# Performance work log

Measured on AMD Instinct MI355X. Metric: run time of the kernel, lower is better.

The kernel has to match this reference:

```python
import jax, jax.numpy as jnp
import numpy as np

B, NB, D, H = 2048, 12, 256, 16
NU, NI, NR = 100000, 100000, 6
EPS = 1e-10


def _lin(k, din, dout):
    k1, k2 = jax.random.split(k)
    s = 1.0 / np.sqrt(din)
    w = jax.random.uniform(k1, (din, dout), minval=-s, maxval=s, dtype=jnp.float32)
    b = jax.random.uniform(k2, (dout,), minval=-s, maxval=s, dtype=jnp.float32)
    return w, b


def setup_inputs() -> dict:
    key = jax.random.key(0)
    ks = jax.random.split(key, 24)
    inp = {}
    inp['iids'] = jax.random.randint(ks[0], (B,), 0, NI)
    inp['i_user_pad'] = jnp.stack([
        jax.random.randint(ks[1], (B, NB), 0, NU),
        jax.random.randint(ks[2], (B, NB), 0, NR)], axis=-1)
    inp['i_item_pad'] = jax.random.randint(ks[3], (B, NB), 0, NI)
    inp['i_item_user_pad'] = jnp.stack([
        jax.random.randint(ks[4], (B, NB, NB), 0, NI),
        jax.random.randint(ks[5], (B, NB, NB), 0, NR)], axis=-1)
    inp['user_table'] = jax.random.normal(ks[6], (NU, D), dtype=jnp.float32) * 0.02
    inp['item_table'] = jax.random.normal(ks[7], (NI, D), dtype=jnp.float32) * 0.02
    inp['rate_table'] = jax.random.normal(ks[8], (NR, D), dtype=jnp.float32) * 0.02
    # g_u: 2D -> D -> D
    inp['g_u_w1'], inp['g_u_b1'] = _lin(ks[9], 2 * D, D)
    inp['g_u_w2'], inp['g_u_b2'] = _lin(ks[10], D, D)
    # item_users_att: 2D -> D -> H
    inp['attu_w1'], inp['attu_b1'] = _lin(ks[11], 2 * D, D)
    inp['attu_w2'], inp['attu_b2'] = _lin(ks[12], D, H)
    # item_users_head: NB*H -> NB*H//2 -> NB
    inp['headu_w1'], inp['headu_b1'] = _lin(ks[13], NB * H, NB * H // 2)
    inp['headu_w2'], inp['headu_b2'] = _lin(ks[14], NB * H // 2, NB)
    # aggre_items: D -> D (+relu)
    inp['aggi_w'], inp['aggi_b'] = _lin(ks[15], D, D)
    # item_items_att: 2D -> D -> H
    inp['attii_w1'], inp['attii_b1'] = _lin(ks[16], 2 * D, D)
    inp['attii_w2'], inp['attii_b2'] = _lin(ks[17], D, H)
    # item_items_head: NB*H -> NB*H//2 -> NB
    inp['headii_w1'], inp['headii_b1'] = _lin(ks[18], NB * H, NB * H // 2)
    inp['headii_w2'], inp['headii_b2'] = _lin(ks[19], NB * H // 2, NB)
    # aggre_item2item: D -> D (+relu)
    inp['aggii_w'], inp['aggii_b'] = _lin(ks[20], D, D)
    # combine_mlp: 2D -> D -> D -> D, relu each
    inp['comb_w1'], inp['comb_b1'] = _lin(ks[21], 2 * D, D)
    inp['comb_w2'], inp['comb_b2'] = _lin(ks[22], D, D)
    inp['comb_w3'], inp['comb_b3'] = _lin(ks[23], D, D)
    return inp


def _mlp(x, w1, b1, w2, b2):
    return jax.nn.relu(x @ w1 + b1) @ w2 + b2


def reference(iids, i_user_pad, i_item_pad, i_item_user_pad,
              user_table, item_table, rate_table,
              g_u_w1, g_u_b1, g_u_w2, g_u_b2,
              attu_w1, attu_b1, attu_w2, attu_b2,
              headu_w1, headu_b1, headu_w2, headu_b2,
              aggi_w, aggi_b,
              attii_w1, attii_b1, attii_w2, attii_b2,
              headii_w1, headii_b1, headii_w2, headii_b2,
              aggii_w, aggii_b,
              comb_w1, comb_b1, comb_w2, comb_b2, comb_w3, comb_b3):
    dt = user_table.dtype
    # ---- stage 1: item <- its users ----
    p_t = user_table[i_user_pad[:, :, 0]]                       # [B,NB,D]
    mask_i = (i_user_pad[:, :, 0] > 0).astype(dt)               # [B,NB]
    er = rate_table[i_user_pad[:, :, 1]]                        # [B,NB,D]
    f_jt = _mlp(jnp.concatenate([p_t, er], -1), g_u_w1, g_u_b1, g_u_w2, g_u_b2)
    q_j = mask_i[:, :, None] * item_table[iids][:, None, :]     # [B,NB,D]
    miu = _mlp(jnp.concatenate([f_jt, q_j], -1), attu_w1, attu_b1, attu_w2, attu_b2)  # [B,NB,H]
    miu = _mlp(miu.reshape(miu.shape[0], -1), headu_w1, headu_b1, headu_w2, headu_b2)  # [B,NB]
    miu = jnp.exp(miu) * mask_i
    miu = miu / (jnp.sum(miu, 1, keepdims=True) + EPS)
    h_jU = jax.nn.relu(jnp.einsum('bn,bnd->bd', miu, f_jt) @ aggi_w + aggi_b)
    # ---- stage 2: neighbor items <- their users ----
    q_a_s = item_table[i_item_user_pad[..., 0]]                 # [B,NB,NB,D]
    mask_s = (i_item_user_pad[..., 0] > 0).astype(dt)           # [B,NB,NB]
    er_s = rate_table[i_item_user_pad[..., 1]]
    x_ia_s = _mlp(jnp.concatenate([q_a_s, er_s], -1), g_u_w1, g_u_b1, g_u_w2, g_u_b2)
    p_i_s = mask_s[..., None] * item_table[i_item_pad][:, :, None, :]
    miu_s = _mlp(jnp.concatenate([x_ia_s, p_i_s], -1), attu_w1, attu_b1, attu_w2, attu_b2)  # [B,NB,NB,H]
    miu_s = _mlp(miu_s.reshape(miu_s.shape[0], miu_s.shape[1], -1),
                 headu_w1, headu_b1, headu_w2, headu_b2)        # [B,NB,NB]
    miu_s = jnp.exp(miu_s) * mask_s
    miu_s = miu_s / (jnp.sum(miu_s, 2, keepdims=True) + EPS)
    h_oU = jax.nn.relu(jnp.einsum('bnm,bnmd->bnd', miu_s, x_ia_s) @ aggi_w + aggi_b)  # [B,NB,D]
    # ---- stage 3: item <- neighbor items ----
    kappa = _mlp(jnp.concatenate([h_oU, item_table[i_item_pad]], -1),
                 attii_w1, attii_b1, attii_w2, attii_b2)        # [B,NB,H]
    kappa = _mlp(kappa.reshape(kappa.shape[0], -1), headii_w1, headii_b1, headii_w2, headii_b2)  # [B,NB]
    mask_su = (i_item_pad > 0).astype(dt)
    kappa = jnp.exp(kappa) * mask_su
    kappa = kappa / (jnp.sum(kappa, 1, keepdims=True) + EPS)
    h_jV = jax.nn.relu(jnp.einsum('bn,bnd->bd', kappa, h_oU) @ aggii_w + aggii_b)
    # ---- combine ----
    h = jnp.concatenate([h_jU, h_jV], 1)
    h = jax.nn.relu(h @ comb_w1 + comb_b1)
    h = jax.nn.relu(h @ comb_w2 + comb_b2)
    return jax.nn.relu(h @ comb_w3 + comb_b3)
```

## Files before the change

kernel.cpp:

```cpp
#include <hip/hip_runtime.h>
#include <cstdint>
#include <cstddef>

typedef short short8 __attribute__((ext_vector_type(8)));
typedef short short4v __attribute__((ext_vector_type(4)));
typedef float f32x4 __attribute__((ext_vector_type(4)));
typedef __bf16 bf16x8 __attribute__((ext_vector_type(8)));

__device__ __forceinline__ unsigned short f2bu(float f) {
  union { float f; unsigned u; } v; v.f = f;
  unsigned r = v.u + 0x7FFFu + ((v.u >> 16) & 1u);
  return (unsigned short)(r >> 16);
}
__device__ __forceinline__ float b2f(unsigned short h) {
  union { unsigned u; float f; } v; v.u = ((unsigned)h) << 16;
  return v.f;
}

__device__ __forceinline__ f32x4 mfma16(short8 a, short8 b, f32x4 c) {
  return __builtin_amdgcn_mfma_f32_16x16x32_bf16(
      __builtin_bit_cast(bf16x8, a), __builtin_bit_cast(bf16x8, b), c, 0, 0, 0);
}

__global__ void k_cvt(const float* __restrict__ in, short* __restrict__ o, int ntot) {
  int i = (blockIdx.x * 256 + threadIdx.x) * 8;
  if (i >= ntot) return;
  float4 a = *(const float4*)(in + i);
  float4 b = *(const float4*)(in + i + 4);
  short8 v;
  v[0] = (short)f2bu(a.x); v[1] = (short)f2bu(a.y);
  v[2] = (short)f2bu(a.z); v[3] = (short)f2bu(a.w);
  v[4] = (short)f2bu(b.x); v[5] = (short)f2bu(b.y);
  v[6] = (short)f2bu(b.z); v[7] = (short)f2bu(b.w);
  *(short8*)(o + i) = v;
}

__global__ void k_cvt_rows(const float* __restrict__ tab, const int* __restrict__ pairs,
                           short* __restrict__ o, int nrows) {
  int t = blockIdx.x * 256 + threadIdx.x;
  if (t >= nrows * 32) return;
  int row = t >> 5;
  int c8 = (t & 31) << 3;
  int id = pairs[2 * row];
  const float* s = tab + (size_t)id * 256 + c8;
  float4 a = *(const float4*)(s);
  float4 b = *(const float4*)(s + 4);
  short8 v;
  v[0] = (short)f2bu(a.x); v[1] = (short)f2bu(a.y);
  v[2] = (short)f2bu(a.z); v[3] = (short)f2bu(a.w);
  v[4] = (short)f2bu(b.x); v[5] = (short)f2bu(b.y);
  v[6] = (short)f2bu(b.z); v[7] = (short)f2bu(b.w);
  *(short8*)(o + (size_t)row * 256 + c8) = v;
}

struct Prep {
  const float* src[16];
  short* dst[16];
  int K[16], N[16], mode[16];
  int boff[17];
};
__global__ void k_prep(Prep p) {
  int b = blockIdx.x, e = 0;
#pragma unroll
  for (int i = 1; i < 16; ++i) if (b >= p.boff[i]) e = i;
  int t = (b - p.boff[e]) * 256 + threadIdx.x;
  const int K = p.K[e], N = p.N[e];
  if (t >= K * N) return;
  const float* w = p.src[e];
  const int m = p.mode[e];
  if (m == 2) { p.dst[e][t] = (short)f2bu(w[t]); return; }
  if (m == 0) {
    int ks = t >> 13, rem = t & 8191;
    int P = rem >> 3, j = rem & 7;
    int n = P >> 2;
    int kq = ((P & 3) - (n >> 1)) & 3;
    int k = (ks << 5) + (kq << 3) + j;
    p.dst[e][t] = (short)f2bu(w[(size_t)k * 256 + n]);
    return;
  }
  int n = t / K, k = t - n * K;
  p.dst[e][t] = (short)f2bu(w[(size_t)k * N + n]);
}

__global__ void k_rc(const float* __restrict__ rate, const float* __restrict__ w1,
                     float* __restrict__ RC) {
  const int j = blockIdx.x;
  const int n = threadIdx.x;
  float s = 0.f;
  const float* rr = rate + j * 256;
  for (int k = 0; k < 256; ++k)
    s += rr[k] * w1[(size_t)(256 + k) * 256 + n];
  RC[j * 256 + n] = s;
}

__global__ __launch_bounds__(256, 4) void k_qc(
    const int* __restrict__ qid, const short* __restrict__ itembf,
    const short* __restrict__ aw1, float* __restrict__ QC)
{
  const int tid = threadIdx.x;
  const int lane = tid & 63;
  const int wave = tid >> 6;
  const int m0 = (int)blockIdx.x << 6;
  const int l15 = lane & 15;
  const int lq = lane >> 4;
  const int nb = wave << 6;

  int pBg[4];
  const short* qp[4];
#pragma unroll
  for (int i = 0; i < 4; ++i) {
    int n = nb + i * 16 + l15;
    pBg[i] = (n * 4 + ((lq + (n >> 1)) & 3)) * 8;
    qp[i] = itembf + (size_t)qid[m0 + i * 16 + l15] * 256 + lq * 8;
  }

  const f32x4 fz = {0.f, 0.f, 0.f, 0.f};
  f32x4 acc[4][4];
#pragma unroll
  for (int ni = 0; ni < 4; ++ni)
#pragma unroll
    for (int mi = 0; mi < 4; ++mi) acc[ni][mi] = fz;

  for (int ks = 0; ks < 8; ++ks) {
    short8 wf[4], qf[4];
#pragma unroll
    for (int i = 0; i < 4; ++i) {
      wf[i] = *(const short8*)(aw1 + (8 + ks) * 8192 + pBg[i]);
      qf[i] = *(const short8*)(qp[i] + ks * 32);
    }
#pragma unroll
    for (int ni = 0; ni < 4; ++ni)
#pragma unroll
      for (int mi = 0; mi < 4; ++mi)
        acc[ni][mi] = mfma16(wf[ni], qf[mi], acc[ni][mi]);
  }
#pragma unroll
  for (int ni = 0; ni < 4; ++ni) {
    const int nbase = nb + ni * 16 + lq * 4;
#pragma unroll
    for (int mi = 0; mi < 4; ++mi) {
      const int m = mi * 16 + l15;
      *(f32x4*)(QC + (size_t)(m0 + m) * 256 + nbase) = acc[ni][mi];
    }
  }
}

template <bool IDENT>
__global__ __launch_bounds__(256, 3) void k_fused(
    const int* __restrict__ idx_pairs,
    const short* __restrict__ tab0,
    const float* __restrict__ RC,
    const float* __restrict__ QC,
    const short* __restrict__ ws1, const float* __restrict__ b1,
    const short* __restrict__ ws2, const float* __restrict__ b2,
    const short* __restrict__ aw1, const float* __restrict__ ab1,
    const short* __restrict__ aw2t, const float* __restrict__ ab2,
    short* __restrict__ Xout, short* __restrict__ miu_out)
{
  __shared__ __align__(16) short smem[20480];
  short* sA0 = smem;
  short* sA1 = smem + 2048;
  short* sH  = smem + 4096;

  const int tid = threadIdx.x;
  const int lane = tid & 63;
  const int wave = tid >> 6;
  const int m0 = (int)blockIdx.x << 6;
  const int l15 = lane & 15;
  const int lq = lane >> 4;
  const int nb = wave << 6;
  const int swz = (l15 & 7) << 3;

  const int an = tid >> 2;
  const int kqA = ((tid & 3) - (an >> 1)) & 3;
  const int r = m0 + an;
  const int i0 = idx_pairs[2 * r];
  const short* a0 = (IDENT ? (tab0 + (size_t)r * 256) : (tab0 + (size_t)i0 * 256)) + kqA * 8;

  int pBg[4], pA[4];
#pragma unroll
  for (int i = 0; i < 4; ++i) {
    int n = nb + i * 16 + l15;
    pBg[i] = (n * 4 + ((lq + (n >> 1)) & 3)) * 8;
    int m = i * 16 + l15;
    pA[i] = (m * 4 + ((lq + (m >> 1)) & 3)) * 8;
  }
  const int hOff = lq * 8;

  const f32x4 fz = {0.f, 0.f, 0.f, 0.f};
  f32x4 acc[4][4];
#pragma unroll
  for (int ni = 0; ni < 4; ++ni)
#pragma unroll
    for (int mi = 0; mi < 4; ++mi) acc[ni][mi] = fz;

  short8 wfb[3][4];
  short8 ar0, ar1;

  int i1v[4], mskv[4], grpv[4];
#pragma unroll
  for (int mi = 0; mi < 4; ++mi) {
    const int row = m0 + mi * 16 + l15;
    i1v[mi]  = idx_pairs[2 * row + 1];
    mskv[mi] = idx_pairs[2 * row];
    grpv[mi] = row / 12;
  }

  {
    short8 t = *(const short8*)a0;
    *(short8*)(sA0 + tid * 8) = t;
  }
  ar1 = *(const short8*)(a0 + 32);
#pragma unroll
  for (int i = 0; i < 4; ++i) wfb[0][i] = *(const short8*)(ws1 + pBg[i]);
#pragma unroll
  for (int i = 0; i < 4; ++i) wfb[1][i] = *(const short8*)(ws1 + 8192 + pBg[i]);
  __syncthreads();
#pragma unroll
  for (int ks = 0; ks < 8; ++ks) {
    short* sAc = (ks & 1) ? sA1 : sA0;
    short* sAn = (ks & 1) ? sA0 : sA1;
    if (ks < 6) {
      const int c = ks + 2;
      short8 t = *(const short8*)(a0 + c * 32);
      if ((ks & 1) == 0) ar0 = t; else ar1 = t;
      const short* s = ws1 + c * 8192;
#pragma unroll
      for (int i = 0; i < 4; ++i) wfb[c % 3][i] = *(const short8*)(s + pBg[i]);
    }
    short8 xf[4];
#pragma unroll
    for (int i = 0; i < 4; ++i) xf[i] = *(short8*)(sAc + pA[i]);
#pragma unroll
    for (int ni = 0; ni < 4; ++ni)
#pragma unroll
      for (int mi = 0; mi < 4; ++mi)
        acc[ni][mi] = mfma16(wfb[ks % 3][ni], xf[mi], acc[ni][mi]);
    if (ks < 7) {
      short8 w = (((ks + 1) & 1) == 0) ? ar0 : ar1;
      *(short8*)(sAn + tid * 8) = w;
      __syncthreads();
    }
  }
#pragma unroll
  for (int ni = 0; ni < 4; ++ni) {
    const int nbase = nb + ni * 16 + lq * 4;
    float4 bb = *(const float4*)(b1 + nbase);
#pragma unroll
    for (int mi = 0; mi < 4; ++mi) {
      const int m = mi * 16 + l15;
      float4 rc = *(const float4*)(RC + i1v[mi] * 256 + nbase);
      short4v hv;
      hv[0] = (short)f2bu(fmaxf(acc[ni][mi][0] + rc.x + bb.x, 0.f));
      hv[1] = (short)f2bu(fmaxf(acc[ni][mi][1] + rc.y + bb.y, 0.f));
      hv[2] = (short)f2bu(fmaxf(acc[ni][mi][2] + rc.z + bb.z, 0.f));
      hv[3] = (short)f2bu(fmaxf(acc[ni][mi][3] + rc.w + bb.w, 0.f));
      *(short4v*)(sH + m * 256 + (nbase ^ swz)) = hv;
    }
  }
  __syncthreads();

#pragma unroll
  for (int ni = 0; ni < 4; ++ni)
#pragma unroll
    for (int mi = 0; mi < 4; ++mi) acc[ni][mi] = fz;
#pragma unroll
  for (int i = 0; i < 4; ++i) wfb[0][i] = *(const short8*)(ws2 + pBg[i]);
#pragma unroll
  for (int i = 0; i < 4; ++i) wfb[1][i] = *(const short8*)(ws2 + 8192 + pBg[i]);
#pragma unroll
  for (int ks = 0; ks < 8; ++ks) {
    if (ks < 6) {
      const short* s = ws2 + (ks + 2) * 8192;
#pragma unroll
      for (int i = 0; i < 4; ++i) wfb[(ks + 2) % 3][i] = *(const short8*)(s + pBg[i]);
    }
    short8 hf[4];
#pragma unroll
    for (int i = 0; i < 4; ++i)
      hf[i] = *(short8*)(sH + (i * 16 + l15) * 256 + ((ks * 32 + hOff) ^ swz));
#pragma unroll
    for (int ni = 0; ni < 4; ++ni)
#pragma unroll
      for (int mi = 0; mi < 4; ++mi)
        acc[ni][mi] = mfma16(wfb[ks % 3][ni], hf[mi], acc[ni][mi]);
  }
  __syncthreads();

#pragma unroll
  for (int ni = 0; ni < 4; ++ni) {
    const int nbase = nb + ni * 16 + lq * 4;
    float4 bb = *(const float4*)(b2 + nbase);
#pragma unroll
    for (int mi = 0; mi < 4; ++mi) {
      const int m = mi * 16 + l15;
      short4v hv;
      hv[0] = (short)f2bu(acc[ni][mi][0] + bb.x);
      hv[1] = (short)f2bu(acc[ni][mi][1] + bb.y);
      hv[2] = (short)f2bu(acc[ni][mi][2] + bb.z);
      hv[3] = (short)f2bu(acc[ni][mi][3] + bb.w);
      *(short4v*)(sH + m * 256 + (nbase ^ swz)) = hv;
      *(short4v*)(Xout + (size_t)(m0 + m) * 256 + nbase) = hv;
    }
  }
  __syncthreads();

#pragma unroll
  for (int ni = 0; ni < 4; ++ni)
#pragma unroll
    for (int mi = 0; mi < 4; ++mi) acc[ni][mi] = fz;
#pragma unroll
  for (int i = 0; i < 4; ++i) wfb[0][i] = *(const short8*)(aw1 + pBg[i]);
#pragma unroll
  for (int i = 0; i < 4; ++i) wfb[1][i] = *(const short8*)(aw1 + 8192 + pBg[i]);
#pragma unroll
  for (int ks = 0; ks < 8; ++ks) {
    if (ks < 6) {
      const short* s = aw1 + (ks + 2) * 8192;
#pragma unroll
      for (int i = 0; i < 4; ++i) wfb[(ks + 2) % 3][i] = *(const short8*)(s + pBg[i]);
    }
    short8 xf[4];
#pragma unroll
    for (int i = 0; i < 4; ++i)
      xf[i] = *(short8*)(sH + (i * 16 + l15) * 256 + ((ks * 32 + hOff) ^ swz));
#pragma unroll
    for (int ni = 0; ni < 4; ++ni)
#pragma unroll
      for (int mi = 0; mi < 4; ++mi)
        acc[ni][mi] = mfma16(wfb[ks % 3][ni], xf[mi], acc[ni][mi]);
  }
  __syncthreads();

#pragma unroll
  for (int ni = 0; ni < 4; ++ni) {
    const int nbase = nb + ni * 16 + lq * 4;
    float4 bb = *(const float4*)(ab1 + nbase);
#pragma unroll
    for (int mi = 0; mi < 4; ++mi) {
      const int m = mi * 16 + l15;
      float4 qv;
      if (mskv[mi] > 0) qv = *(const float4*)(QC + (size_t)grpv[mi] * 256 + nbase);
      else { qv.x = 0.f; qv.y = 0.f; qv.z = 0.f; qv.w = 0.f; }
      short4v hv;
      hv[0] = (short)f2bu(fmaxf(acc[ni][mi][0] + qv.x + bb.x, 0.f));
      hv[1] = (short)f2bu(fmaxf(acc[ni][mi][1] + qv.y + bb.y, 0.f));
      hv[2] = (short)f2bu(fmaxf(acc[ni][mi][2] + qv.z + bb.z, 0.f));
      hv[3] = (short)f2bu(fmaxf(acc[ni][mi][3] + qv.w + bb.w, 0.f));
      *(short4v*)(sH + m * 256 + (nbase ^ swz)) = hv;
    }
  }
  __syncthreads();

  f32x4 a2 = fz;
#pragma unroll
  for (int ks = 0; ks < 8; ++ks) {
    short8 af = *(short8*)(sH + (wave * 16 + l15) * 256 + ((ks * 32 + hOff) ^ swz));
    short8 bv = *(const short8*)(aw2t + l15 * 256 + ks * 32 + hOff);
    a2 = mfma16(af, bv, a2);
  }
  const float bias = ab2[l15];
#pragma unroll
  for (int j = 0; j < 4; ++j)
    miu_out[(size_t)(m0 + wave * 16 + lq * 4 + j) * 16 + l15] = (short)f2bu(a2[j] + bias);
}

__global__ __launch_bounds__(256, 3) void k_attonly(
    const short* __restrict__ first,
    const short* __restrict__ itembf,
    const int* __restrict__ iidx,
    const short* __restrict__ aw1, const float* __restrict__ ab1,
    const short* __restrict__ aw2t, const float* __restrict__ ab2,
    short* __restrict__ out)
{
  __shared__ __align__(16) short sH[16896];

  const int tid = threadIdx.x;
  const int lane = tid & 63;
  const int wave = tid >> 6;
  const int m0 = (int)blockIdx.x << 6;
  const int l15 = lane & 15;
  const int lq = lane >> 4;
  const int nb = wave << 6;
  const int hOff = lq * 8;

  const short* fp[4];
  const short* qp[4];
  int pBg[4];
#pragma unroll
  for (int i = 0; i < 4; ++i) {
    int mrow = m0 + i * 16 + l15;
    fp[i] = first + (size_t)mrow * 256 + hOff;
    qp[i] = itembf + (size_t)iidx[mrow] * 256 + hOff;
    int n = nb + i * 16 + l15;
    pBg[i] = (n * 4 + ((lq + (n >> 1)) & 3)) * 8;
  }

  const f32x4 fz = {0.f, 0.f, 0.f, 0.f};
  f32x4 acc[4][4];
#pragma unroll
  for (int ni = 0; ni < 4; ++ni)
#pragma unroll
    for (int mi = 0; mi < 4; ++mi) acc[ni][mi] = fz;

  short8 wfc[4], wfn[4], xfc[4], xfn[4];
#pragma unroll
  for (int i = 0; i < 4; ++i) {
    wfc[i] = *(const short8*)(aw1 + pBg[i]);
    xfc[i] = *(const short8*)(fp[i]);
  }
  for (int ks = 0; ks < 16; ++ks) {
    if (ks < 15) {
      const int c = ks + 1;
      const short* s = aw1 + c * 8192;
#pragma unroll
      for (int i = 0; i < 4; ++i) {
        wfn[i] = *(const short8*)(s + pBg[i]);
        xfn[i] = *(const short8*)((c < 8) ? (fp[i] + c * 32) : (qp[i] + (c - 8) * 32));
      }
    }
#pragma unroll
    for (int ni = 0; ni < 4; ++ni)
#pragma unroll
      for (int mi = 0; mi < 4; ++mi)
        acc[ni][mi] = mfma16(wfc[ni], xfc[mi], acc[ni][mi]);
    if (ks < 15) {
#pragma unroll
      for (int i = 0; i < 4; ++i) { wfc[i] = wfn[i]; xfc[i] = xfn[i]; }
    }
  }
#pragma unroll
  for (int ni = 0; ni < 4; ++ni) {
    const int nbase = nb + ni * 16 + lq * 4;
    float4 bb = *(const float4*)(ab1 + nbase);
#pragma unroll
    for (int mi = 0; mi < 4; ++mi) {
      const int m = mi * 16 + l15;
      short4v hv;
      hv[0] = (short)f2bu(fmaxf(acc[ni][mi][0] + bb.x, 0.f));
      hv[1] = (short)f2bu(fmaxf(acc[ni][mi][1] + bb.y, 0.f));
      hv[2] = (short)f2bu(fmaxf(acc[ni][mi][2] + bb.z, 0.f));
      hv[3] = (short)f2bu(fmaxf(acc[ni][mi][3] + bb.w, 0.f));
      *(short4v*)(sH + m * 264 + nbase) = hv;
    }
  }
  __syncthreads();
  f32x4 a2 = fz;
#pragma unroll
  for (int ks = 0; ks < 8; ++ks) {
    short8 af = *(short8*)(sH + (wave * 16 + l15) * 264 + ks * 32 + hOff);
    short8 bv = *(const short8*)(aw2t + l15 * 256 + ks * 32 + hOff);
    a2 = mfma16(af, bv, a2);
  }
  const float bias = ab2[l15];
#pragma unroll
  for (int j = 0; j < 4; ++j)
    out[(size_t)(m0 + wave * 16 + lq * 4 + j) * 16 + l15] = (short)f2bu(a2[j] + bias);
}

__global__ __launch_bounds__(256, 3) void k_gemm1(
    const short* __restrict__ Abf, const short* __restrict__ wt,
    const float* __restrict__ bias, short* __restrict__ out)
{
  const int tid  = threadIdx.x;
  const int lane = tid & 63;
  const int wave = tid >> 6;
  const int m0   = blockIdx.x << 6;
  const int l15  = lane & 15;
  const int lq   = lane >> 4;
  const int rq   = lq << 2;
  const int nb   = wave << 6;
  const int hOff = lq * 8;

  const f32x4 fz = {0.f, 0.f, 0.f, 0.f};
  f32x4 acc[4][4];
#pragma unroll
  for (int mi = 0; mi < 4; ++mi)
#pragma unroll
    for (int ni = 0; ni < 4; ++ni) acc[mi][ni] = fz;

  for (int ks = 0; ks < 8; ++ks) {
    short8 af[4], bv[4];
#pragma unroll
    for (int i = 0; i < 4; ++i) {
      af[i] = *(const short8*)(Abf + (size_t)(m0 + i * 16 + l15) * 256 + ks * 32 + hOff);
      bv[i] = *(const short8*)(wt + (size_t)(nb + i * 16 + l15) * 256 + ks * 32 + hOff);
    }
#pragma unroll
    for (int mi = 0; mi < 4; ++mi)
#pragma unroll
      for (int ni = 0; ni < 4; ++ni)
        acc[mi][ni] = mfma16(af[mi], bv[ni], acc[mi][ni]);
  }

#pragma unroll
  for (int ni = 0; ni < 4; ++ni) {
    const int col = nb + ni * 16 + l15;
    const float b = bias[col];
#pragma unroll
    for (int mi = 0; mi < 4; ++mi)
#pragma unroll
      for (int j = 0; j < 4; ++j) {
        const int row = mi * 16 + rq + j;
        out[(size_t)(m0 + row) * 256 + col] = (short)f2bu(fmaxf(acc[mi][ni][j] + b, 0.f));
      }
  }
}

__global__ __launch_bounds__(256, 2) void k_comb(
    const short* __restrict__ hju, const short* __restrict__ hjv,
    const short* __restrict__ w1t, const float* __restrict__ b1,
    const short* __restrict__ w2t, const float* __restrict__ b2,
    const short* __restrict__ w3t, const float* __restrict__ b3,
    float* __restrict__ out)
{
  __shared__ __align__(16) short smem[29696];
  short (*A)[40]   = (short(*)[40])smem;
  short (*Bt)[40]  = (short(*)[40])(smem + 2560);
  short (*Hh)[264] = (short(*)[264])(smem + 12800);

  const int tid  = threadIdx.x;
  const int lane = tid & 63;
  const int wave = tid >> 6;
  const int m0   = blockIdx.x << 6;
  const int arow = tid >> 2;
  const int acol8 = (tid & 3) << 3;
  const int lrow = lane & 15;
  const int lk8  = (lane >> 4) << 3;
  const int rq   = (lane >> 4) << 2;
  const int nb   = wave << 6;
  const int r = m0 + arow;

  const f32x4 fz = {0.f, 0.f, 0.f, 0.f};
  f32x4 acc[4][4];
#pragma unroll
  for (int mi = 0; mi < 4; ++mi)
#pragma unroll
    for (int ni = 0; ni < 4; ++ni) acc[mi][ni] = fz;

  for (int ks = 0; ks < 16; ++ks) {
    const int kg = (ks << 5) + acol8;
    short8 av = (kg < 256) ? *(const short8*)(hju + (size_t)r * 256 + kg)
                           : *(const short8*)(hjv + (size_t)r * 256 + (kg - 256));
    *(short8*)&A[arow][acol8] = av;
    const short* wsrc = w1t + tid * 512 + (ks << 5);
    *(short8*)&Bt[tid][0]  = *(const short8*)(wsrc);
    *(short8*)&Bt[tid][8]  = *(const short8*)(wsrc + 8);
    *(short8*)&Bt[tid][16] = *(const short8*)(wsrc + 16);
    *(short8*)&Bt[tid][24] = *(const short8*)(wsrc + 24);
    __syncthreads();
    short8 af[4], bv[4];
#pragma unroll
    for (int mi = 0; mi < 4; ++mi) af[mi] = *(short8*)&A[mi * 16 + lrow][lk8];
#pragma unroll
    for (int ni = 0; ni < 4; ++ni) bv[ni] = *(short8*)&Bt[nb + ni * 16 + lrow][lk8];
#pragma unroll
    for (int mi = 0; mi < 4; ++mi)
#pragma unroll
      for (int ni = 0; ni < 4; ++ni)
        acc[mi][ni] = mfma16(af[mi], bv[ni], acc[mi][ni]);
    __syncthreads();
  }
#pragma unroll
  for (int ni = 0; ni < 4; ++ni) {
    const int col = nb + ni * 16 + lrow;
    const float bias = b1[col];
#pragma unroll
    for (int mi = 0; mi < 4; ++mi)
#pragma unroll
      for (int j = 0; j < 4; ++j)
        Hh[mi * 16 + rq + j][col] = (short)f2bu(fmaxf(acc[mi][ni][j] + bias, 0.f));
  }

#pragma unroll
  for (int mi = 0; mi < 4; ++mi)
#pragma unroll
    for (int ni = 0; ni < 4; ++ni) acc[mi][ni] = fz;
  for (int ks = 0; ks < 8; ++ks) {
    const short* wsrc = w2t + tid * 256 + (ks << 5);
    *(short8*)&Bt[tid][0]  = *(const short8*)(wsrc);
    *(short8*)&Bt[tid][8]  = *(const short8*)(wsrc + 8);
    *(short8*)&Bt[tid][16] = *(const short8*)(wsrc + 16);
    *(short8*)&Bt[tid][24] = *(const short8*)(wsrc + 24);
    __syncthreads();
    short8 af[4], bv[4];
#pragma unroll
    for (int mi = 0; mi < 4; ++mi) af[mi] = *(short8*)&Hh[mi * 16 + lrow][(ks << 5) + lk8];
#pragma unroll
    for (int ni = 0; ni < 4; ++ni) bv[ni] = *(short8*)&Bt[nb + ni * 16 + lrow][lk8];
#pragma unroll
    for (int mi = 0; mi < 4; ++mi)
#pragma unroll
      for (int ni = 0; ni < 4; ++ni)
        acc[mi][ni] = mfma16(af[mi], bv[ni], acc[mi][ni]);
    __syncthreads();
  }
#pragma unroll
  for (int ni = 0; ni < 4; ++ni) {
    const int col = nb + ni * 16 + lrow;
    const float bias = b2[col];
#pragma unroll
    for (int mi = 0; mi < 4; ++mi)
#pragma unroll
      for (int j = 0; j < 4; ++j)
        Hh[mi * 16 + rq + j][col] = (short)f2bu(fmaxf(acc[mi][ni][j] + bias, 0.f));
  }
  __syncthreads();

#pragma unroll
  for (int mi = 0; mi < 4; ++mi)
#pragma unroll
    for (int ni = 0; ni < 4; ++ni) acc[mi][ni] = fz;
  for (int ks = 0; ks < 8; ++ks) {
    const short* wsrc = w3t + tid * 256 + (ks << 5);
    *(short8*)&Bt[tid][0]  = *(const short8*)(wsrc);
    *(short8*)&Bt[tid][8]  = *(const short8*)(wsrc + 8);
    *(short8*)&Bt[tid][16] = *(const short8*)(wsrc + 16);
    *(short8*)&Bt[tid][24] = *(const short8*)(wsrc + 24);
    __syncthreads();
    short8 af[4], bv[4];
#pragma unroll
    for (int mi = 0; mi < 4; ++mi) af[mi] = *(short8*)&Hh[mi * 16 + lrow][(ks << 5) + lk8];
#pragma unroll
    for (int ni = 0; ni < 4; ++ni) bv[ni] = *(short8*)&Bt[nb + ni * 16 + lrow][lk8];
#pragma unroll
    for (int mi = 0; mi < 4; ++mi)
#pragma unroll
      for (int ni = 0; ni < 4; ++ni)
        acc[mi][ni] = mfma16(af[mi], bv[ni], acc[mi][ni]);
    __syncthreads();
  }
#pragma unroll
  for (int ni = 0; ni < 4; ++ni) {
    const int col = nb + ni * 16 + lrow;
    const float bias = b3[col];
#pragma unroll
    for (int mi = 0; mi < 4; ++mi)
#pragma unroll
      for (int j = 0; j < 4; ++j) {
        const int row = mi * 16 + rq + j;
        out[(size_t)(m0 + row) * 256 + col] = fmaxf(acc[mi][ni][j] + bias, 0.f);
      }
  }
}

__global__ __launch_bounds__(256, 4) void k_h1(
    const short* __restrict__ A, const short* __restrict__ w1t,
    const float* __restrict__ b1, short* __restrict__ h1)
{
  const int tid = threadIdx.x;
  const int lane = tid & 63;
  const int wave = tid >> 6;
  const int m0 = (int)blockIdx.x << 6;
  const int l15 = lane & 15;
  const int lq = lane >> 4;
  const int ntc = (wave < 2) ? 2 : 1;
  const int nta = wave;
  const int ntb = wave + 4;

  const f32x4 fz = {0.f, 0.f, 0.f, 0.f};
  f32x4 acc[4][2];
#pragma unroll
  for (int i = 0; i < 4; ++i) { acc[i][0] = fz; acc[i][1] = fz; }

  for (int ks = 0; ks < 6; ++ks) {
    short8 af[4], bv[2];
#pragma unroll
    for (int i = 0; i < 4; ++i)
      af[i] = *(const short8*)(A + (size_t)(m0 + i * 16 + l15) * 192 + ks * 32 + lq * 8);
    bv[0] = *(const short8*)(w1t + (nta * 16 + l15) * 192 + ks * 32 + lq * 8);
    if (ntc == 2)
      bv[1] = *(const short8*)(w1t + (ntb * 16 + l15) * 192 + ks * 32 + lq * 8);
#pragma unroll
    for (int j = 0; j < 2; ++j)
      if (j < ntc)
#pragma unroll
        for (int i = 0; i < 4; ++i)
          acc[i][j] = mfma16(bv[j], af[i], acc[i][j]);
  }
#pragma unroll
  for (int j = 0; j < 2; ++j) {
    if (j >= ntc) continue;
    const int nbase = (j == 0 ? nta : ntb) * 16 + lq * 4;
    float4 bb = *(const float4*)(b1 + nbase);
#pragma unroll
    for (int i = 0; i < 4; ++i) {
      const int row = m0 + i * 16 + l15;
      short4v hv;
      hv[0] = (short)f2bu(fmaxf(acc[i][j][0] + bb.x, 0.f));
      hv[1] = (short)f2bu(fmaxf(acc[i][j][1] + bb.y, 0.f));
      hv[2] = (short)f2bu(fmaxf(acc[i][j][2] + bb.z, 0.f));
      hv[3] = (short)f2bu(fmaxf(acc[i][j][3] + bb.w, 0.f));
      *(short4v*)(h1 + (size_t)row * 96 + nbase) = hv;
    }
  }
}

__global__ __launch_bounds__(256) void k_h2(
    const short* __restrict__ h1, const short* __restrict__ w2t,
    const float* __restrict__ b2,
    const int* __restrict__ mask_src, const int mstride,
    float* __restrict__ W)
{
  __shared__ float wgt[16][12];
  const int tid = threadIdx.x;
  const int gg = tid >> 4, sl = tid & 15;
  const int g = blockIdx.x * 16 + gg;
  if (sl < 12) {
    float s = b2[sl];
    const short* hr = h1 + (size_t)g * 96;
    const short* wr = w2t + sl * 96;
#pragma unroll
    for (int kk = 0; kk < 12; ++kk) {
      short8 hv = *(const short8*)(hr + kk * 8);
      short8 wv = *(const short8*)(wr + kk * 8);
#pragma unroll
      for (int j = 0; j < 8; ++j)
        s += b2f((unsigned short)hv[j]) * b2f((unsigned short)wv[j]);
    }
    const int mi = mask_src[(g * 12 + sl) * mstride];
    wgt[gg][sl] = (mi > 0) ? expf(s) : 0.f;
  }
  __syncthreads();
  if (sl < 12) {
    float tot = 1e-10f;
#pragma unroll
    for (int m = 0; m < 12; ++m) tot += wgt[gg][m];
    W[(size_t)g * 12 + sl] = wgt[gg][sl] / tot;
  }
}

__global__ __launch_bounds__(256) void k_wsum(
    const float* __restrict__ W, const short* __restrict__ X,
    short* __restrict__ out)
{
  const int tid = threadIdx.x;
  const int g = blockIdx.x * 8 + (tid >> 5);
  const int d0 = (tid & 31) * 8;
  const float* wg = W + (size_t)g * 12;
  float w[12];
#pragma unroll
  for (int m = 0; m < 12; ++m) w[m] = wg[m];
  const short* xp = X + (size_t)g * 12 * 256 + d0;
  float o[8];
#pragma unroll
  for (int j = 0; j < 8; ++j) o[j] = 0.f;
#pragma unroll
  for (int m = 0; m < 12; ++m) {
    short8 x = *(const short8*)(xp + m * 256);
#pragma unroll
    for (int j = 0; j < 8; ++j) o[j] += w[m] * b2f((unsigned short)x[j]);
  }
  short8 v;
#pragma unroll
  for (int j = 0; j < 8; ++j) v[j] = (short)f2bu(o[j]);
  *(short8*)(out + (size_t)g * 256 + d0) = v;
}

extern "C" void kernel_launch(void* const* d_in, const int* in_sizes, int n_in,
                              void* d_out, int out_size, void* d_ws, size_t ws_size,
                              hipStream_t stream)
{
  (void)in_sizes; (void)n_in; (void)out_size; (void)ws_size;

  const int*   iids = (const int*)d_in[0];
  const int*   iup  = (const int*)d_in[1];
  const int*   iip  = (const int*)d_in[2];
  const int*   iiup = (const int*)d_in[3];
  const float* user_table = (const float*)d_in[4];
  const float* item_table = (const float*)d_in[5];
  const float* rate_table = (const float*)d_in[6];
  const float* g_u_w1 = (const float*)d_in[7];   const float* g_u_b1 = (const float*)d_in[8];
  const float* g_u_w2 = (const float*)d_in[9];   const float* g_u_b2 = (const float*)d_in[10];
  const float* attu_w1 = (const float*)d_in[11]; const float* attu_b1 = (const float*)d_in[12];
  const float* attu_w2 = (const float*)d_in[13]; const float* attu_b2 = (const float*)d_in[14];
  const float* headu_w1 = (const float*)d_in[15]; const float* headu_b1 = (const float*)d_in[16];
  const float* headu_w2 = (const float*)d_in[17]; const float* headu_b2 = (const float*)d_in[18];
  const float* aggi_w = (const float*)d_in[19];  const float* aggi_b = (const float*)d_in[20];
  const float* attii_w1 = (const float*)d_in[21]; const float* attii_b1 = (const float*)d_in[22];
  const float* attii_w2 = (const float*)d_in[23]; const float* attii_b2 = (const float*)d_in[24];
  const float* headii_w1 = (const float*)d_in[25]; const float* headii_b1 = (const float*)d_in[26];
  const float* headii_w2 = (const float*)d_in[27]; const float* headii_b2 = (const float*)d_in[28];
  const float* aggii_w = (const float*)d_in[29]; const float* aggii_b = (const float*)d_in[30];
  const float* comb_w1 = (const float*)d_in[31]; const float* comb_b1 = (const float*)d_in[32];
  const float* comb_w2 = (const float*)d_in[33]; const float* comb_b2 = (const float*)d_in[34];
  const float* comb_w3 = (const float*)d_in[35]; const float* comb_b3 = (const float*)d_in[36];

  const int NIe = 100000 * 256;
  const int M2 = 2048 * 12 * 12;
  const int M1 = 2048 * 12;
  const int G2 = M1;
  const int G1 = 2048;

  char* wsp = (char*)d_ws;
  size_t off = 0;
  auto alloc = [&](size_t bytes) -> void* {
    void* p = wsp + off;
    off += (bytes + 255) & ~(size_t)255;
    return p;
  };
  short* item_bf = (short*)alloc((size_t)NIe * 2);
  short* urows   = (short*)alloc((size_t)M1 * 256 * 2);
  short* sl_gu1   = (short*)alloc((size_t)512 * 256 * 2);
  short* sl_gu2   = (short*)alloc((size_t)256 * 256 * 2);
  short* sl_attu1 = (short*)alloc((size_t)512 * 256 * 2);
  short* sl_attii1= (short*)alloc((size_t)512 * 256 * 2);
  short* wt_attu2 = (short*)alloc((size_t)256 * 16 * 2);
  short* wt_attii2= (short*)alloc((size_t)256 * 16 * 2);
  short* wt_aggi   = (short*)alloc((size_t)256 * 256 * 2);
  short* wt_aggii  = (short*)alloc((size_t)256 * 256 * 2);
  short* wt_comb1  = (short*)alloc((size_t)512 * 256 * 2);
  short* wt_comb2  = (short*)alloc((size_t)256 * 256 * 2);
  short* wt_comb3  = (short*)alloc((size_t)256 * 256 * 2);
  short* hu1t  = (short*)alloc((size_t)96 * 192 * 2);
  short* hu2t  = (short*)alloc((size_t)12 * 96 * 2);
  short* hii1t = (short*)alloc((size_t)96 * 192 * 2);
  short* hii2t = (short*)alloc((size_t)12 * 96 * 2);
  float* RC    = (float*)alloc((size_t)6 * 256 * 4);
  float* QC2   = (float*)alloc((size_t)G2 * 256 * 4);
  float* QC1   = (float*)alloc((size_t)G1 * 256 * 4);

  short* X      = (short*)alloc((size_t)M2 * 256 * 2);
  short* FJT    = (short*)alloc((size_t)M1 * 256 * 2);
  short* MIU2   = (short*)alloc((size_t)M2 * 16 * 2);
  short* MIU1   = (short*)alloc((size_t)M1 * 16 * 2);
  short* KAP    = (short*)alloc((size_t)M1 * 16 * 2);
  short* H1A    = (short*)alloc((size_t)G2 * 96 * 2);
  short* H1K    = (short*)alloc((size_t)G1 * 96 * 2);
  short* H1M    = (short*)alloc((size_t)G1 * 96 * 2);
  float* WA     = (float*)alloc((size_t)G2 * 12 * 4);
  float* WK     = (float*)alloc((size_t)G1 * 12 * 4);
  float* WM     = (float*)alloc((size_t)G1 * 12 * 4);
  short* HPRE2  = (short*)alloc((size_t)M1 * 256 * 2);
  short* HOU    = (short*)alloc((size_t)M1 * 256 * 2);
  short* HPREJV = (short*)alloc((size_t)2048 * 256 * 2);
  short* HPRE1  = (short*)alloc((size_t)2048 * 256 * 2);
  short* HJU    = (short*)alloc((size_t)2048 * 256 * 2);
  short* HJV    = (short*)alloc((size_t)2048 * 256 * 2);

  k_cvt<<<NIe / 8 / 256, 256, 0, stream>>>(item_table, item_bf, NIe);
  k_cvt_rows<<<(M1 * 32) / 256, 256, 0, stream>>>(user_table, iup, urows, M1);
  k_rc<<<6, 256, 0, stream>>>(rate_table, g_u_w1, RC);

  Prep pp;
  int nbk = 0, ei = 0;
  auto addw = [&](const float* s, short* d, int K, int N, int mode) {
    pp.src[ei] = s; pp.dst[ei] = d; pp.K[ei] = K; pp.N[ei] = N; pp.mode[ei] = mode;
    pp.boff[ei] = nbk; nbk += (K * N + 255) / 256; ++ei;
  };
  addw(g_u_w1,   sl_gu1,    512, 256, 0);
  addw(g_u_w2,   sl_gu2,    256, 256, 0);
  addw(attu_w1,  sl_attu1,  512, 256, 0);
  addw(attii_w1, sl_attii1, 512, 256, 0);
  addw(attu_w2,  wt_attu2,  256, 16, 1);
  addw(attii_w2, wt_attii2, 256, 16, 1);
  addw(aggi_w,   wt_aggi,   256, 256, 1);
  addw(aggii_w,  wt_aggii,  256, 256, 1);
  addw(comb_w1,  wt_comb1,  512, 256, 1);
  addw(comb_w2,  wt_comb2,  256, 256, 1);
  addw(comb_w3,  wt_comb3,  256, 256, 1);
  addw(headu_w1,  hu1t,  192, 96, 1);
  addw(headu_w2,  hu2t,  96, 12, 1);
  addw(headii_w1, hii1t, 192, 96, 1);
  addw(headii_w2, hii2t, 96, 12, 1);
  pp.boff[15] = nbk;
  pp.boff[16] = nbk;
  k_prep<<<nbk, 256, 0, stream>>>(pp);

  k_qc<<<G2 / 64, 256, 0, stream>>>(iip, item_bf, sl_attu1, QC2);
  k_qc<<<G1 / 64, 256, 0, stream>>>(iids, item_bf, sl_attu1, QC1);

  k_fused<false><<<M2 / 64, 256, 0, stream>>>(iiup, item_bf, RC, QC2,
                                              sl_gu1, g_u_b1, sl_gu2, g_u_b2,
                                              sl_attu1, attu_b1, wt_attu2, attu_b2,
                                              X, MIU2);
  k_fused<true><<<M1 / 64, 256, 0, stream>>>(iup, urows, RC, QC1,
                                             sl_gu1, g_u_b1, sl_gu2, g_u_b2,
                                             sl_attu1, attu_b1, wt_attu2, attu_b2,
                                             FJT, MIU1);

  k_h1<<<G2 / 64, 256, 0, stream>>>(MIU2, hu1t, headu_b1, H1A);
  k_h2<<<G2 / 16, 256, 0, stream>>>(H1A, hu2t, headu_b2, iiup, 2, WA);
  k_wsum<<<G2 / 8, 256, 0, stream>>>(WA, X, HPRE2);

  k_gemm1<<<M1 / 64, 256, 0, stream>>>(HPRE2, wt_aggi, aggi_b, HOU);
  k_attonly<<<M1 / 64, 256, 0, stream>>>(HOU, item_bf, iip,
                                         sl_attii1, attii_b1, wt_attii2, attii_b2, KAP);

  k_h1<<<G1 / 64, 256, 0, stream>>>(KAP, hii1t, headii_b1, H1K);
  k_h2<<<G1 / 16, 256, 0, stream>>>(H1K, hii2t, headii_b2, iip, 1, WK);
  k_wsum<<<G1 / 8, 256, 0, stream>>>(WK, HOU, HPREJV);

  k_h1<<<G1 / 64, 256, 0, stream>>>(MIU1, hu1t, headu_b1, H1M);
  k_h2<<<G1 / 16, 256, 0, stream>>>(H1M, hu2t, headu_b2, iup, 2, WM);
  k_wsum<<<G1 / 8, 256, 0, stream>>>(WM, FJT, HPRE1);

  k_gemm1<<<2048 / 64, 256, 0, stream>>>(HPRE1, wt_aggi, aggi_b, HJU);
  k_gemm1<<<2048 / 64, 256, 0, stream>>>(HPREJV, wt_aggii, aggii_b, HJV);
  k_comb<<<2048 / 64, 256, 0, stream>>>(HJU, HJV, wt_comb1, comb_b1,
                                        wt_comb2, comb_b2, wt_comb3, comb_b3,
                                        (float*)d_out);
}
```

Measured before the change: 509.1 us.

## Fuse attention head MLP, softmax and weighted sum into the main fused kernel

The fused gather+MLP kernel now processes 48 rows (four groups of 12 neighbors) per block instead of 64. This lets each block finish the per-group head MLP, masked exp-normalisation and weighted sum of the X features itself, keeping everything in shared memory. It removes the global writes of X/MIU and the separate k_h1, k_h2 and k_wsum launches for both the item-user and user paths. The cost is a smaller MFMA tile (3 instead of 4 row fragments), a single-buffered A stage with an extra barrier per k-step, more shared memory per block, and scalar per-lane head dot products.

```diff
diff --git a/kernel.cpp b/kernel.cpp
--- a/kernel.cpp
+++ b/kernel.cpp
@@ -146,7 +146,7 @@
 }
 
 template <bool IDENT>
-__global__ __launch_bounds__(256, 3) void k_fused(
+__global__ __launch_bounds__(256, 3) void k_fused2(
     const int* __restrict__ idx_pairs,
     const short* __restrict__ tab0,
     const float* __restrict__ RC,
@@ -155,62 +155,68 @@
     const short* __restrict__ ws2, const float* __restrict__ b2,
     const short* __restrict__ aw1, const float* __restrict__ ab1,
     const short* __restrict__ aw2t, const float* __restrict__ ab2,
-    short* __restrict__ Xout, short* __restrict__ miu_out)
+    const short* __restrict__ h1t, const float* __restrict__ hb1,
+    const short* __restrict__ h2t, const float* __restrict__ hb2,
+    short* __restrict__ HPRE)
 {
-  __shared__ __align__(16) short smem[20480];
-  short* sA0 = smem;
-  short* sA1 = smem + 2048;
-  short* sH  = smem + 4096;
+  __shared__ __align__(16) short smem[26112];
+  short* sA = smem;
+  short* sS = smem;
+  short* h1d = smem + 768;
+  float* wgt = (float*)(smem + 1152);
+  short* sH = smem + 1536;
+  short* sF = smem + 13824;
 
   const int tid = threadIdx.x;
   const int lane = tid & 63;
   const int wave = tid >> 6;
-  const int m0 = (int)blockIdx.x << 6;
+  const int m0 = (int)blockIdx.x * 48;
   const int l15 = lane & 15;
   const int lq = lane >> 4;
   const int nb = wave << 6;
   const int swz = (l15 & 7) << 3;
 
-  const int an = tid >> 2;
+  const int an = (tid < 192) ? (tid >> 2) : 0;
   const int kqA = ((tid & 3) - (an >> 1)) & 3;
-  const int r = m0 + an;
-  const int i0 = idx_pairs[2 * r];
-  const short* a0 = (IDENT ? (tab0 + (size_t)r * 256) : (tab0 + (size_t)i0 * 256)) + kqA * 8;
-
-  int pBg[4], pA[4];
+  const int rA0 = m0 + an;
+  const int i0s = idx_pairs[2 * rA0];
+  const short* a0 = (IDENT ? (tab0 + (size_t)rA0 * 256) : (tab0 + (size_t)i0s * 256)) + kqA * 8;
+
+  int pBg[4], pA[3];
 #pragma unroll
   for (int i = 0; i < 4; ++i) {
     int n = nb + i * 16 + l15;
     pBg[i] = (n * 4 + ((lq + (n >> 1)) & 3)) * 8;
+  }
+#pragma unroll
+  for (int i = 0; i < 3; ++i) {
     int m = i * 16 + l15;
     pA[i] = (m * 4 + ((lq + (m >> 1)) & 3)) * 8;
   }
   const int hOff = lq * 8;
 
   const f32x4 fz = {0.f, 0.f, 0.f, 0.f};
-  f32x4 acc[4][4];
+  f32x4 acc[4][3];
 #pragma unroll
   for (int ni = 0; ni < 4; ++ni)
 #pragma unroll
-    for (int mi = 0; mi < 4; ++mi) acc[ni][mi] = fz;
+    for (int mi = 0; mi < 3; ++mi) acc[ni][mi] = fz;
 
   short8 wfb[3][4];
-  short8 ar0, ar1;
-
-  int i1v[4], mskv[4], grpv[4];
-#pragma unroll
-  for (int mi = 0; mi < 4; ++mi) {
+  short8 rAr;
+
+  int i1v[3], mskv[3], grpv[3];
+#pragma unroll
+  for (int mi = 0; mi < 3; ++mi) {
     const int row = m0 + mi * 16 + l15;
     i1v[mi]  = idx_pairs[2 * row + 1];
     mskv[mi] = idx_pairs[2 * row];
     grpv[mi] = row / 12;
   }
 
-  {
-    short8 t = *(const short8*)a0;
-    *(short8*)(sA0 + tid * 8) = t;
-  }
-  ar1 = *(const short8*)(a0 + 32);
+  rAr = *(const short8*)a0;
+  if (tid < 192) *(short8*)(sA + tid * 8) = rAr;
+  rAr = *(const short8*)(a0 + 32);
 #pragma unroll
   for (int i = 0; i < 4; ++i) wfb[0][i] = *(const short8*)(ws1 + pBg[i]);
 #pragma unroll
@@ -218,27 +224,23 @@
   __syncthreads();
 #pragma unroll
   for (int ks = 0; ks < 8; ++ks) {
-    short* sAc = (ks & 1) ? sA1 : sA0;
-    short* sAn = (ks & 1) ? sA0 : sA1;
     if (ks < 6) {
-      const int c = ks + 2;
-      short8 t = *(const short8*)(a0 + c * 32);
-      if ((ks & 1) == 0) ar0 = t; else ar1 = t;
-      const short* s = ws1 + c * 8192;
-#pragma unroll
-      for (int i = 0; i < 4; ++i) wfb[c % 3][i] = *(const short8*)(s + pBg[i]);
-    }
-    short8 xf[4];
-#pragma unroll
-    for (int i = 0; i < 4; ++i) xf[i] = *(short8*)(sAc + pA[i]);
+      const short* s = ws1 + (ks + 2) * 8192;
+#pragma unroll
+      for (int i = 0; i < 4; ++i) wfb[(ks + 2) % 3][i] = *(const short8*)(s + pBg[i]);
+    }
+    short8 xf[3];
+#pragma unroll
+    for (int i = 0; i < 3; ++i) xf[i] = *(short8*)(sA + pA[i]);
 #pragma unroll
     for (int ni = 0; ni < 4; ++ni)
 #pragma unroll
-      for (int mi = 0; mi < 4; ++mi)
+      for (int mi = 0; mi < 3; ++mi)
         acc[ni][mi] = mfma16(wfb[ks % 3][ni], xf[mi], acc[ni][mi]);
     if (ks < 7) {
-      short8 w = (((ks + 1) & 1) == 0) ? ar0 : ar1;
-      *(short8*)(sAn + tid * 8) = w;
+      __syncthreads();
+      if (tid < 192) *(short8*)(sA + tid * 8) = rAr;
+      if (ks < 6) rAr = *(const short8*)(a0 + (ks + 2) * 32);
       __syncthreads();
     }
   }
@@ -247,7 +249,7 @@
     const int nbase = nb + ni * 16 + lq * 4;
     float4 bb = *(const float4*)(b1 + nbase);
 #pragma unroll
-    for (int mi = 0; mi < 4; ++mi) {
+    for (int mi = 0; mi < 3; ++mi) {
       const int m = mi * 16 + l15;
       float4 rc = *(const float4*)(RC + i1v[mi] * 256 + nbase);
       short4v hv;
@@ -263,7 +265,7 @@
 #pragma unroll
   for (int ni = 0; ni < 4; ++ni)
 #pragma unroll
-    for (int mi = 0; mi < 4; ++mi) acc[ni][mi] = fz;
+    for (int mi = 0; mi < 3; ++mi) acc[ni][mi] = fz;
 #pragma unroll
   for (int i = 0; i < 4; ++i) wfb[0][i] = *(const short8*)(ws2 + pBg[i]);
 #pragma unroll
@@ -275,14 +277,14 @@
 #pragma unroll
       for (int i = 0; i < 4; ++i) wfb[(ks + 2) % 3][i] = *(const short8*)(s + pBg[i]);
     }
-    short8 hf[4];
-#pragma unroll
-    for (int i = 0; i < 4; ++i)
+    short8 hf[3];
+#pragma unroll
+    for (int i = 0; i < 3; ++i)
       hf[i] = *(short8*)(sH + (i * 16 + l15) * 256 + ((ks * 32 + hOff) ^ swz));
 #pragma unroll
     for (int ni = 0; ni < 4; ++ni)
 #pragma unroll
-      for (int mi = 0; mi < 4; ++mi)
+      for (int mi = 0; mi < 3; ++mi)
         acc[ni][mi] = mfma16(wfb[ks % 3][ni], hf[mi], acc[ni][mi]);
   }
   __syncthreads();
@@ -292,7 +294,7 @@
     const int nbase = nb + ni * 16 + lq * 4;
     float4 bb = *(const float4*)(b2 + nbase);
 #pragma unroll
-    for (int mi = 0; mi < 4; ++mi) {
+    for (int mi = 0; mi < 3; ++mi) {
       const int m = mi * 16 + l15;
       short4v hv;
       hv[0] = (short)f2bu(acc[ni][mi][0] + bb.x);
@@ -300,7 +302,7 @@
       hv[2] = (short)f2bu(acc[ni][mi][2] + bb.z);
       hv[3] = (short)f2bu(acc[ni][mi][3] + bb.w);
       *(short4v*)(sH + m * 256 + (nbase ^ swz)) = hv;
-      *(short4v*)(Xout + (size_t)(m0 + m) * 256 + nbase) = hv;
+      *(short4v*)(sF + m * 256 + nbase) = hv;
     }
   }
   __syncthreads();
@@ -308,7 +310,7 @@
 #pragma unroll
   for (int ni = 0; ni < 4; ++ni)
 #pragma unroll
-    for (int mi = 0; mi < 4; ++mi) acc[ni][mi] = fz;
+    for (int mi = 0; mi < 3; ++mi) acc[ni][mi] = fz;
 #pragma unroll
   for (int i = 0; i < 4; ++i) wfb[0][i] = *(const short8*)(aw1 + pBg[i]);
 #pragma unroll
@@ -320,14 +322,14 @@
 #pragma unroll
       for (int i = 0; i < 4; ++i) wfb[(ks + 2) % 3][i] = *(const short8*)(s + pBg[i]);
     }
-    short8 xf[4];
-#pragma unroll
-    for (int i = 0; i < 4; ++i)
+    short8 xf[3];
+#pragma unroll
+    for (int i = 0; i < 3; ++i)
       xf[i] = *(short8*)(sH + (i * 16 + l15) * 256 + ((ks * 32 + hOff) ^ swz));
 #pragma unroll
     for (int ni = 0; ni < 4; ++ni)
 #pragma unroll
-      for (int mi = 0; mi < 4; ++mi)
+      for (int mi = 0; mi < 3; ++mi)
         acc[ni][mi] = mfma16(wfb[ks % 3][ni], xf[mi], acc[ni][mi]);
   }
   __syncthreads();
@@ -337,7 +339,7 @@
     const int nbase = nb + ni * 16 + lq * 4;
     float4 bb = *(const float4*)(ab1 + nbase);
 #pragma unroll
-    for (int mi = 0; mi < 4; ++mi) {
+    for (int mi = 0; mi < 3; ++mi) {
       const int m = mi * 16 + l15;
       float4 qv;
       if (mskv[mi] > 0) qv = *(const float4*)(QC + (size_t)grpv[mi] * 256 + nbase);
@@ -352,17 +354,79 @@
   }
   __syncthreads();
 
-  f32x4 a2 = fz;
-#pragma unroll
-  for (int ks = 0; ks < 8; ++ks) {
-    short8 af = *(short8*)(sH + (wave * 16 + l15) * 256 + ((ks * 32 + hOff) ^ swz));
-    short8 bv = *(const short8*)(aw2t + l15 * 256 + ks * 32 + hOff);
-    a2 = mfma16(af, bv, a2);
-  }
-  const float bias = ab2[l15];
-#pragma unroll
-  for (int j = 0; j < 4; ++j)
-    miu_out[(size_t)(m0 + wave * 16 + lq * 4 + j) * 16 + l15] = (short)f2bu(a2[j] + bias);
+  if (wave < 3) {
+    f32x4 a2 = fz;
+#pragma unroll
+    for (int ks = 0; ks < 8; ++ks) {
+      short8 af = *(short8*)(sH + (wave * 16 + l15) * 256 + ((ks * 32 + hOff) ^ swz));
+      short8 bv = *(const short8*)(aw2t + l15 * 256 + ks * 32 + hOff);
+      a2 = mfma16(af, bv, a2);
+    }
+    const float bias = ab2[l15];
+#pragma unroll
+    for (int j = 0; j < 4; ++j)
+      sS[(wave * 16 + lq * 4 + j) * 16 + l15] = (short)f2bu(a2[j] + bias);
+  }
+  __syncthreads();
+
+  const int gi = m0 / 12 + wave;
+#pragma unroll
+  for (int jj = 0; jj < 2; ++jj) {
+    const int j = lane + jj * 64;
+    if (j < 96) {
+      float s = hb1[j];
+      const short* wr = h1t + j * 192;
+      const short* sv = sS + wave * 192;
+#pragma unroll
+      for (int k = 0; k < 192; k += 8) {
+        short8 wv = *(const short8*)(wr + k);
+        short8 xv = *(const short8*)(sv + k);
+#pragma unroll
+        for (int q = 0; q < 8; ++q)
+          s += b2f((unsigned short)xv[q]) * b2f((unsigned short)wv[q]);
+      }
+      h1d[wave * 96 + j] = (short)f2bu(fmaxf(s, 0.f));
+    }
+  }
+  if (lane < 12) {
+    float z = hb2[lane];
+    const short* hr = h1d + wave * 96;
+    const short* wr = h2t + lane * 96;
+#pragma unroll
+    for (int k = 0; k < 96; k += 8) {
+      short8 hv = *(const short8*)(hr + k);
+      short8 wv = *(const short8*)(wr + k);
+#pragma unroll
+      for (int q = 0; q < 8; ++q)
+        z += b2f((unsigned short)hv[q]) * b2f((unsigned short)wv[q]);
+    }
+    const int msk = idx_pairs[2 * (gi * 12 + lane)];
+    wgt[wave * 12 + lane] = (msk > 0) ? expf(z) : 0.f;
+  }
+  if (lane < 12) {
+    float tot = 1e-10f;
+#pragma unroll
+    for (int m = 0; m < 12; ++m) tot += wgt[wave * 12 + m];
+    wgt[wave * 12 + lane] = wgt[wave * 12 + lane] / tot;
+  }
+
+  {
+    float o0 = 0.f, o1 = 0.f, o2 = 0.f, o3 = 0.f;
+    const int c0 = lane * 4;
+#pragma unroll
+    for (int m = 0; m < 12; ++m) {
+      const float wm = wgt[wave * 12 + m];
+      short4v x = *(short4v*)(sF + (wave * 12 + m) * 256 + c0);
+      o0 += wm * b2f((unsigned short)x[0]);
+      o1 += wm * b2f((unsigned short)x[1]);
+      o2 += wm * b2f((unsigned short)x[2]);
+      o3 += wm * b2f((unsigned short)x[3]);
+    }
+    short4v ov;
+    ov[0] = (short)f2bu(o0); ov[1] = (short)f2bu(o1);
+    ov[2] = (short)f2bu(o2); ov[3] = (short)f2bu(o3);
+    *(short4v*)(HPRE + (size_t)gi * 256 + c0) = ov;
+  }
 }
 
 __global__ __launch_bounds__(256, 3) void k_attonly(
@@ -820,18 +884,10 @@
   float* QC2   = (float*)alloc((size_t)G2 * 256 * 4);
   float* QC1   = (float*)alloc((size_t)G1 * 256 * 4);
 
-  short* X      = (short*)alloc((size_t)M2 * 256 * 2);
-  short* FJT    = (short*)alloc((size_t)M1 * 256 * 2);
-  short* MIU2   = (short*)alloc((size_t)M2 * 16 * 2);
-  short* MIU1   = (short*)alloc((size_t)M1 * 16 * 2);
   short* KAP    = (short*)alloc((size_t)M1 * 16 * 2);
-  short* H1A    = (short*)alloc((size_t)G2 * 96 * 2);
   short* H1K    = (short*)alloc((size_t)G1 * 96 * 2);
-  short* H1M    = (short*)alloc((size_t)G1 * 96 * 2);
-  float* WA     = (float*)alloc((size_t)G2 * 12 * 4);
   float* WK     = (float*)alloc((size_t)G1 * 12 * 4);
-  float* WM     = (float*)alloc((size_t)G1 * 12 * 4);
-  short* HPRE2  = (short*)alloc((size_t)M1 * 256 * 2);
+  short* HPRE2  = (short*)alloc((size_t)G2 * 256 * 2);
   short* HOU    = (short*)alloc((size_t)M1 * 256 * 2);
   short* HPREJV = (short*)alloc((size_t)2048 * 256 * 2);
   short* HPRE1  = (short*)alloc((size_t)2048 * 256 * 2);
@@ -870,18 +926,16 @@
   k_qc<<<G2 / 64, 256, 0, stream>>>(iip, item_bf, sl_attu1, QC2);
   k_qc<<<G1 / 64, 256, 0, stream>>>(iids, item_bf, sl_attu1, QC1);
 
-  k_fused<false><<<M2 / 64, 256, 0, stream>>>(iiup, item_bf, RC, QC2,
+  k_fused2<false><<<M2 / 48, 256, 0, stream>>>(iiup, item_bf, RC, QC2,
+                                               sl_gu1, g_u_b1, sl_gu2, g_u_b2,
+                                               sl_attu1, attu_b1, wt_attu2, attu_b2,
+                                               hu1t, headu_b1, hu2t, headu_b2,
+                                               HPRE2);
+  k_fused2<true><<<M1 / 48, 256, 0, stream>>>(iup, urows, RC, QC1,
                                               sl_gu1, g_u_b1, sl_gu2, g_u_b2,
                                               sl_attu1, attu_b1, wt_attu2, attu_b2,
-                                              X, MIU2);
-  k_fused<true><<<M1 / 64, 256, 0, stream>>>(iup, urows, RC, QC1,
-                                             sl_gu1, g_u_b1, sl_gu2, g_u_b2,
-                                             sl_attu1, attu_b1, wt_attu2, attu_b2,
-                                             FJT, MIU1);
-
-  k_h1<<<G2 / 64, 256, 0, stream>>>(MIU2, hu1t, headu_b1, H1A);
-  k_h2<<<G2 / 16, 256, 0, stream>>>(H1A, hu2t, headu_b2, iiup, 2, WA);
-  k_wsum<<<G2 / 8, 256, 0, stream>>>(WA, X, HPRE2);
+                                              hu1t, headu_b1, hu2t, headu_b2,
+                                              HPRE1);
 
   k_gemm1<<<M1 / 64, 256, 0, stream>>>(HPRE2, wt_aggi, aggi_b, HOU);
   k_attonly<<<M1 / 64, 256, 0, stream>>>(HOU, item_bf, iip,
@@ -890,10 +944,6 @@
   k_h1<<<G1 / 64, 256, 0, stream>>>(KAP, hii1t, headii_b1, H1K);
   k_h2<<<G1 / 16, 256, 0, stream>>>(H1K, hii2t, headii_b2, iip, 1, WK);
   k_wsum<<<G1 / 8, 256, 0, stream>>>(WK, HOU, HPREJV);
-
-  k_h1<<<G1 / 64, 256, 0, stream>>>(MIU1, hu1t, headu_b1, H1M);
-  k_h2<<<G1 / 16, 256, 0, stream>>>(H1M, hu2t, headu_b2, iup, 2, WM);
-  k_wsum<<<G1 / 8, 256, 0, stream>>>(WM, FJT, HPRE1);
 
   k_gemm1<<<2048 / 64, 256, 0, stream>>>(HPRE1, wt_aggi, aggi_b, HJU);
   k_gemm1<<<2048 / 64, 256, 0, stream>>>(HPREJV, wt_aggii, aggii_b, HJV);
```

Measured after the change: 525.2 us. 1.03x slower.
